# Performance work log

Measured on AMD Instinct MI355X. Metric: run time of the kernel, lower is better.

## Reference

```python
import jax, jax.numpy as jnp
import numpy as np
from jax import lax

B, S = 64, 256          # batch, max sentence length
D, H = 1024, 1024       # encoder hidden (input_dim), LSTM hidden_dim
E, O = 128, 512         # embedding_dim, output_dim (label vocab)
IN = D + E              # lstm_input_dim = input_dim + embedding_dim


def setup_inputs() -> dict:
    key = jax.random.key(0)
    ks = jax.random.split(key, 10)
    u = 1.0 / np.sqrt(H)  # torch LSTM/Linear init scale
    return {
        "hidden": jax.random.normal(ks[0], (B, S, D), jnp.float32),
        "init_tensor": jax.random.normal(ks[1], (1, E), jnp.float32),
        "emb_table": jax.random.normal(ks[2], (O, E), jnp.float32),
        "w_ih": jax.random.uniform(ks[3], (4 * H, IN), jnp.float32, -u, u),
        "w_hh": jax.random.uniform(ks[4], (4 * H, H), jnp.float32, -u, u),
        "b_ih": jax.random.uniform(ks[5], (4 * H,), jnp.float32, -u, u),
        "b_hh": jax.random.uniform(ks[6], (4 * H,), jnp.float32, -u, u),
        "w_out": jax.random.uniform(ks[7], (O, H), jnp.float32, -u, u),
        "b_out": jax.random.uniform(ks[8], (O,), jnp.float32, -u, u),
        "seq_lens": jax.random.randint(ks[9], (B,), 1, S + 1, jnp.int32),
    }


def reference(hidden, init_tensor, emb_table, w_ih, w_hh, b_ih, b_hh,
              w_out, b_out, seq_lens):
    """Autoregressive branch of Seq2SeqDecoder (no teacher forcing):
    per-step LSTM cell -> linear -> argmax -> embedding feedback.
    Dropout is identity (rate 0 / eval). Returns padded [B, S, O] logits,
    zeroed past seq_lens (matching flat2matrix zero padding).
    """
    b = b_ih + b_hh

    def step(carry, x_t):
        h, c, prev_emb = carry                 # [B,H],[B,H],[B,E]
        inp = jnp.concatenate([x_t, prev_emb], axis=-1)       # [B, D+E]
        gates = inp @ w_ih.T + h @ w_hh.T + b                 # [B, 4H]
        i, f, g, o = jnp.split(gates, 4, axis=-1)             # torch gate order
        i, f, o = jax.nn.sigmoid(i), jax.nn.sigmoid(f), jax.nn.sigmoid(o)
        g = jnp.tanh(g)
        c_new = f * c + i * g
        h_new = o * jnp.tanh(c_new)
        logits = h_new @ w_out.T + b_out                      # [B, O]
        idx = jnp.argmax(logits, axis=-1)                     # topk(1)
        return (h_new, c_new, emb_table[idx]), logits

    h0 = jnp.zeros((B, H), hidden.dtype)
    c0 = jnp.zeros((B, H), hidden.dtype)
    e0 = jnp.broadcast_to(init_tensor, (B, E))
    init = (h0, c0, e0)
    _, logits = lax.scan(step, init, jnp.swapaxes(hidden, 0, 1))  # [S,B,O]
    logits = jnp.swapaxes(logits, 0, 1)                            # [B,S,O]
    mask = jnp.arange(S)[None, :] < seq_lens[:, None]              # [B,S]
    return jnp.where(mask[:, :, None], logits, 0.0)
```

## Files before the change

### kernel.cpp

```cpp
#include <hip/hip_runtime.h>
#include <hip/hip_bf16.h>
#include <math.h>

#define B_  64
#define S_  256
#define D_  1024
#define H_  1024
#define E_  128
#define O_  512
#define IN_ 1152
#define G4_ 4096
#define KU_ 1152
#define KS_ 8

__global__ __launch_bounds__(256) void k_init(
    const float* __restrict__ init_tensor,
    const float* __restrict__ w_out,
    float* __restrict__ u, float* __restrict__ c,
    float* __restrict__ w_out_T)
{
  const int NU = B_ * KU_;
  const int NC = B_ * H_;
  const int NT = H_ * O_;
  const int total = NU + NC + NT;
  for (int idx = blockIdx.x * 256 + threadIdx.x; idx < total; idx += gridDim.x * 256) {
    if (idx < NU) {
      int k = idx % KU_;
      u[idx] = (k < E_) ? init_tensor[k] : 0.f;
    } else if (idx < NU + NC) {
      c[idx - NU] = 0.f;
    } else {
      int i = idx - NU - NC;
      int o = i >> 10, k = i & 1023;
      w_out_T[k * O_ + o] = w_out[i];
    }
  }
}

__global__ __launch_bounds__(256) void k_xw(
    const float* __restrict__ hidden,
    const float* __restrict__ w_ih,
    const float* __restrict__ b_ih,
    const float* __restrict__ b_hh,
    float* __restrict__ xwb, int t0, int rows)
{
  __shared__ float a_t[16][132];
  __shared__ float b_t[16][132];
  const int tid = threadIdx.x;
  const int tx = tid & 15, ty = tid >> 4;
  const int m_base = blockIdx.x * 128;
  const int n_base = blockIdx.y * 128;
  float acc[8][8];
#pragma unroll
  for (int i = 0; i < 8; ++i)
#pragma unroll
    for (int j = 0; j < 8; ++j) acc[i][j] = 0.f;

  for (int k0 = 0; k0 < D_; k0 += 16) {
#pragma unroll
    for (int l = 0; l < 2; ++l) {
      int s = tid + l * 256;
      int r = s >> 2, kq = (s & 3) << 2;
      int m = m_base + r;
      float4 v = make_float4(0.f, 0.f, 0.f, 0.f);
      if (m < rows) {
        int t = t0 + (m >> 6), b = m & 63;
        v = *(const float4*)(hidden + ((size_t)b * S_ + t) * D_ + k0 + kq);
      }
      a_t[kq + 0][r] = v.x; a_t[kq + 1][r] = v.y; a_t[kq + 2][r] = v.z; a_t[kq + 3][r] = v.w;
      int j = n_base + r;
      float4 w = *(const float4*)(w_ih + (size_t)j * IN_ + k0 + kq);
      b_t[kq + 0][r] = w.x; b_t[kq + 1][r] = w.y; b_t[kq + 2][r] = w.z; b_t[kq + 3][r] = w.w;
    }
    __syncthreads();
#pragma unroll
    for (int k = 0; k < 16; ++k) {
      float av[8], bv[8];
      *(float4*)&av[0] = *(const float4*)&a_t[k][ty * 4];
      *(float4*)&av[4] = *(const float4*)&a_t[k][64 + ty * 4];
      *(float4*)&bv[0] = *(const float4*)&b_t[k][tx * 4];
      *(float4*)&bv[4] = *(const float4*)&b_t[k][64 + tx * 4];
#pragma unroll
      for (int i = 0; i < 8; ++i)
#pragma unroll
        for (int j = 0; j < 8; ++j)
          acc[i][j] = fmaf(av[i], bv[j], acc[i][j]);
    }
    __syncthreads();
  }
  float bias[8];
#pragma unroll
  for (int cj = 0; cj < 8; ++cj) {
    int col = n_base + ((cj < 4) ? (tx * 4 + cj) : (64 + tx * 4 + cj - 4));
    bias[cj] = b_ih[col] + b_hh[col];
  }
#pragma unroll
  for (int ri = 0; ri < 8; ++ri) {
    int m = m_base + ((ri < 4) ? (ty * 4 + ri) : (64 + ty * 4 + ri - 4));
    if (m < rows) {
      float4 s0 = make_float4(acc[ri][0] + bias[0], acc[ri][1] + bias[1],
                              acc[ri][2] + bias[2], acc[ri][3] + bias[3]);
      float4 s1 = make_float4(acc[ri][4] + bias[4], acc[ri][5] + bias[5],
                              acc[ri][6] + bias[6], acc[ri][7] + bias[7]);
      *(float4*)(xwb + (size_t)m * G4_ + n_base + tx * 4) = s0;
      *(float4*)(xwb + (size_t)m * G4_ + n_base + 64 + tx * 4) = s1;
    }
  }
}

__global__ __launch_bounds__(256) void k_gates(
    const float* __restrict__ u,
    const float* __restrict__ w_ih,
    const float* __restrict__ w_hh,
    float* __restrict__ gp)
{
  __shared__ float u_t[48][68];
  __shared__ float w_t[48][68];
  const int jt = blockIdx.x;
  const int ks = blockIdx.y;
  const int tid = threadIdx.x;
  const int tx = tid & 15, ty = tid >> 4;
  const int j_base = jt * 64;
  float acc[4][4];
#pragma unroll
  for (int i = 0; i < 4; ++i)
#pragma unroll
    for (int j = 0; j < 4; ++j) acc[i][j] = 0.f;

  for (int sub = 0; sub < 3; ++sub) {
    const int k0 = ks * 144 + sub * 48;
#pragma unroll
    for (int l = 0; l < 3; ++l) {
      int s = tid + l * 256;
      int row = s / 12;
      int kq = (s % 12) * 4;
      float4 v = *(const float4*)(u + (size_t)row * KU_ + k0 + kq);
      u_t[kq + 0][row] = v.x; u_t[kq + 1][row] = v.y; u_t[kq + 2][row] = v.z; u_t[kq + 3][row] = v.w;
      int kg = k0 + kq;
      int j = j_base + row;
      const float* src = (kg < E_) ? (w_ih + (size_t)j * IN_ + D_ + kg)
                                   : (w_hh + (size_t)j * H_ + (kg - E_));
      float4 w = *(const float4*)src;
      w_t[kq + 0][row] = w.x; w_t[kq + 1][row] = w.y; w_t[kq + 2][row] = w.z; w_t[kq + 3][row] = w.w;
    }
    __syncthreads();
#pragma unroll 16
    for (int k = 0; k < 48; ++k) {
      float uv[4], wv[4];
      *(float4*)uv = *(const float4*)&u_t[k][ty * 4];
      *(float4*)wv = *(const float4*)&w_t[k][tx * 4];
#pragma unroll
      for (int i = 0; i < 4; ++i)
#pragma unroll
        for (int j = 0; j < 4; ++j)
          acc[i][j] = fmaf(uv[i], wv[j], acc[i][j]);
    }
    __syncthreads();
  }
#pragma unroll
  for (int i = 0; i < 4; ++i) {
    int b = ty * 4 + i;
    *(float4*)(gp + ((size_t)ks * B_ + b) * G4_ + j_base + tx * 4) =
        make_float4(acc[i][0], acc[i][1], acc[i][2], acc[i][3]);
  }
}

__global__ __launch_bounds__(256) void k_cell(
    const float* __restrict__ xwb,
    const float* __restrict__ gp,
    float* __restrict__ u,
    float* __restrict__ c,
    const float* __restrict__ w_out_T,
    float* __restrict__ lp,
    int trel)
{
  __shared__ float h_lds[8][128];
  const int bg = blockIdx.x & 7;
  const int sl = blockIdx.x >> 3;
  const int tid = threadIdx.x;
#pragma unroll
  for (int r = 0; r < 4; ++r) {
    int p = tid + r * 256;
    int bl = p >> 7, jjl = p & 127;
    int b = bg * 8 + bl;
    int jj = sl * 128 + jjl;
    float g4[4];
#pragma unroll
    for (int g = 0; g < 4; ++g) {
      int j = g * H_ + jj;
      float v = xwb[((size_t)trel * B_ + b) * G4_ + j];
#pragma unroll
      for (int s8 = 0; s8 < 8; ++s8)
        v += gp[((size_t)s8 * B_ + b) * G4_ + j];
      g4[g] = v;
    }
    float iv = 1.f / (1.f + expf(-g4[0]));
    float fv = 1.f / (1.f + expf(-g4[1]));
    float gv = tanhf(g4[2]);
    float ov = 1.f / (1.f + expf(-g4[3]));
    float cc = fv * c[(size_t)b * H_ + jj] + iv * gv;
    c[(size_t)b * H_ + jj] = cc;
    float hv = ov * tanhf(cc);
    u[(size_t)b * KU_ + E_ + jj] = hv;
    h_lds[bl][jjl] = hv;
  }
  __syncthreads();
  float a0[8], a1[8];
#pragma unroll
  for (int bl = 0; bl < 8; ++bl) { a0[bl] = 0.f; a1[bl] = 0.f; }
  for (int kc = 0; kc < 128; kc += 4) {
    float hb[8][4];
#pragma unroll
    for (int bl = 0; bl < 8; ++bl)
      *(float4*)hb[bl] = *(const float4*)&h_lds[bl][kc];
#pragma unroll
    for (int kk = 0; kk < 4; ++kk) {
      int krow = sl * 128 + kc + kk;
      float w0 = w_out_T[(size_t)krow * O_ + tid];
      float w1 = w_out_T[(size_t)krow * O_ + tid + 256];
#pragma unroll
      for (int bl = 0; bl < 8; ++bl) {
        a0[bl] = fmaf(hb[bl][kk], w0, a0[bl]);
        a1[bl] = fmaf(hb[bl][kk], w1, a1[bl]);
      }
    }
  }
#pragma unroll
  for (int bl = 0; bl < 8; ++bl) {
    int b = bg * 8 + bl;
    lp[((size_t)sl * B_ + b) * O_ + tid]       = a0[bl];
    lp[((size_t)sl * B_ + b) * O_ + tid + 256] = a1[bl];
  }
}

__global__ __launch_bounds__(256) void k_amax(
    const float* __restrict__ lp,
    const float* __restrict__ b_out,
    const float* __restrict__ emb_table,
    const int* __restrict__ seq_lens,
    float* __restrict__ u,
    float* __restrict__ out,
    int t)
{
  __shared__ float sv[256];
  __shared__ int   si[256];
  const int b = blockIdx.x;
  const int tid = threadIdx.x;
  float v0 = b_out[tid];
  float v1 = b_out[tid + 256];
#pragma unroll
  for (int sl = 0; sl < 8; ++sl) {
    v0 += lp[((size_t)sl * B_ + b) * O_ + tid];
    v1 += lp[((size_t)sl * B_ + b) * O_ + tid + 256];
  }
  int len = seq_lens[b];
  float* orow = out + ((size_t)b * S_ + t) * O_;
  bool live = (t < len);
  orow[tid]       = live ? v0 : 0.f;
  orow[tid + 256] = live ? v1 : 0.f;
  float bv = (v1 > v0) ? v1 : v0;
  int   bi = (v1 > v0) ? (tid + 256) : tid;
  sv[tid] = bv; si[tid] = bi;
  __syncthreads();
  for (int s = 128; s > 0; s >>= 1) {
    if (tid < s) {
      float ov = sv[tid + s]; int oi = si[tid + s];
      if (ov > sv[tid] || (ov == sv[tid] && oi < si[tid])) { sv[tid] = ov; si[tid] = oi; }
    }
    __syncthreads();
  }
  int idx = si[0];
  if (tid < E_) u[(size_t)b * KU_ + tid] = emb_table[(size_t)idx * E_ + tid];
}

extern "C" void kernel_launch(void* const* d_in, const int* in_sizes, int n_in,
                              void* d_out, int out_size, void* d_ws, size_t ws_size,
                              hipStream_t stream) {
  const float* hidden      = (const float*)d_in[0];
  const float* init_tensor = (const float*)d_in[1];
  const float* emb_table   = (const float*)d_in[2];
  const float* w_ih        = (const float*)d_in[3];
  const float* w_hh        = (const float*)d_in[4];
  const float* b_ih        = (const float*)d_in[5];
  const float* b_hh        = (const float*)d_in[6];
  const float* w_out       = (const float*)d_in[7];
  const float* b_out       = (const float*)d_in[8];
  const int*   seq_lens    = (const int*)d_in[9];
  float* out = (float*)d_out;
  float* ws  = (float*)d_ws;

  const size_t U_OFF  = 0;
  const size_t C_OFF  = U_OFF + (size_t)B_ * KU_;
  const size_t GP_OFF = C_OFF + (size_t)B_ * H_;
  const size_t LP_OFF = GP_OFF + (size_t)KS_ * B_ * G4_;
  const size_t WT_OFF = LP_OFF + (size_t)8 * B_ * O_;
  const size_t XW_OFF = WT_OFF + (size_t)H_ * O_;

  long long avail = (long long)(ws_size / 4) - (long long)XW_OFF;
  long long chl = avail / ((long long)B_ * G4_);
  int CH = (int)(chl < 1 ? 1 : (chl > S_ ? S_ : chl));

  k_init<<<dim3(2592), dim3(256), 0, stream>>>(init_tensor, w_out,
                                               ws + U_OFF, ws + C_OFF, ws + WT_OFF);

  for (int t0 = 0; t0 < S_; t0 += CH) {
    int ch = (S_ - t0 < CH) ? (S_ - t0) : CH;
    int rows = ch * B_;
    dim3 pg((rows + 127) / 128, G4_ / 128);
    k_xw<<<pg, dim3(256), 0, stream>>>(hidden, w_ih, b_ih, b_hh, ws + XW_OFF, t0, rows);
    for (int t = t0; t < t0 + ch; ++t) {
      k_gates<<<dim3(64, KS_), dim3(256), 0, stream>>>(ws + U_OFF, w_ih, w_hh, ws + GP_OFF);
      k_cell<<<dim3(64), dim3(256), 0, stream>>>(ws + XW_OFF, ws + GP_OFF, ws + U_OFF,
                                                 ws + C_OFF, ws + WT_OFF, ws + LP_OFF, t - t0);
      k_amax<<<dim3(B_), dim3(256), 0, stream>>>(ws + LP_OFF, b_out, emb_table, seq_lens,
                                                 ws + U_OFF, out, t);
    }
  }
}
```

Measured before the change: 10.40 ms.

## Replace per-step kernel launches with persistent cooperative kernel holding weights in registers

Merges the three per-timestep kernels (gates GEMM, LSTM cell + output projection, argmax + embedding feedback) into one persistent cooperative kernel that loops over timesteps and uses grid.sync between phases. Each block keeps its slice of the recurrent and output weights in registers for the whole sequence, so they are not re-read from memory every step, and the state is stored batch-interleaved in LDS-friendly layout. This removes about 768 kernel launches and the repeated weight traffic, at the cost of two grid-wide barriers per step and heavy register and LDS use, which forces a fixed 256-block, 512-thread launch with two blocks per CU.

```diff
diff --git a/kernel.cpp b/kernel.cpp
--- a/kernel.cpp
+++ b/kernel.cpp
@@ -1,6 +1,9 @@
 #include <hip/hip_runtime.h>
 #include <hip/hip_bf16.h>
+#include <hip/hip_cooperative_groups.h>
 #include <math.h>
+
+namespace cg = cooperative_groups;
 
 #define B_  64
 #define S_  256
@@ -11,28 +14,21 @@
 #define IN_ 1152
 #define G4_ 4096
 #define KU_ 1152
-#define KS_ 8
+#define KW_ 144
+
 
 __global__ __launch_bounds__(256) void k_init(
     const float* __restrict__ init_tensor,
-    const float* __restrict__ w_out,
-    float* __restrict__ u, float* __restrict__ c,
-    float* __restrict__ w_out_T)
+    float* __restrict__ u_g, float* __restrict__ c_g)
 {
-  const int NU = B_ * KU_;
-  const int NC = B_ * H_;
-  const int NT = H_ * O_;
-  const int total = NU + NC + NT;
-  for (int idx = blockIdx.x * 256 + threadIdx.x; idx < total; idx += gridDim.x * 256) {
+  const int NU = 4 * KU_ * 16;
+  const int NC = H_ * B_;
+  for (int idx = blockIdx.x * 256 + threadIdx.x; idx < NU + NC; idx += gridDim.x * 256) {
     if (idx < NU) {
-      int k = idx % KU_;
-      u[idx] = (k < E_) ? init_tensor[k] : 0.f;
-    } else if (idx < NU + NC) {
-      c[idx - NU] = 0.f;
+      int k = (idx >> 4) % KU_;
+      u_g[idx] = (k < E_) ? init_tensor[k] : 0.f;
     } else {
-      int i = idx - NU - NC;
-      int o = i >> 10, k = i & 1023;
-      w_out_T[k * O_ + o] = w_out[i];
+      c_g[idx - NU] = 0.f;
     }
   }
 }
@@ -108,169 +104,162 @@
   }
 }
 
-__global__ __launch_bounds__(256) void k_gates(
-    const float* __restrict__ u,
-    const float* __restrict__ w_ih,
-    const float* __restrict__ w_hh,
-    float* __restrict__ gp)
+__global__ __launch_bounds__(512, 2) void k_steps(
+    const float* __restrict__ w_ih, const float* __restrict__ w_hh,
+    const float* __restrict__ w_out, const float* __restrict__ b_out,
+    const float* __restrict__ emb_table, const int* __restrict__ seq_lens,
+    const float* __restrict__ xwb,
+    float* __restrict__ u_g, float* __restrict__ c_g, float* __restrict__ lp,
+    float* __restrict__ out, int t0, int nsteps)
 {
-  __shared__ float u_t[48][68];
-  __shared__ float w_t[48][68];
-  const int jt = blockIdx.x;
-  const int ks = blockIdx.y;
-  const int tid = threadIdx.x;
-  const int tx = tid & 15, ty = tid >> 4;
-  const int j_base = jt * 64;
-  float acc[4][4];
-#pragma unroll
-  for (int i = 0; i < 4; ++i)
-#pragma unroll
-    for (int j = 0; j < 4; ++j) acc[i][j] = 0.f;
-
-  for (int sub = 0; sub < 3; ++sub) {
-    const int k0 = ks * 144 + sub * 48;
-#pragma unroll
-    for (int l = 0; l < 3; ++l) {
-      int s = tid + l * 256;
-      int row = s / 12;
-      int kq = (s % 12) * 4;
-      float4 v = *(const float4*)(u + (size_t)row * KU_ + k0 + kq);
-      u_t[kq + 0][row] = v.x; u_t[kq + 1][row] = v.y; u_t[kq + 2][row] = v.z; u_t[kq + 3][row] = v.w;
-      int kg = k0 + kq;
-      int j = j_base + row;
-      const float* src = (kg < E_) ? (w_ih + (size_t)j * IN_ + D_ + kg)
-                                   : (w_hh + (size_t)j * H_ + (kg - E_));
-      float4 w = *(const float4*)src;
-      w_t[kq + 0][row] = w.x; w_t[kq + 1][row] = w.y; w_t[kq + 2][row] = w.z; w_t[kq + 3][row] = w.w;
-    }
-    __syncthreads();
-#pragma unroll 16
-    for (int k = 0; k < 48; ++k) {
-      float uv[4], wv[4];
-      *(float4*)uv = *(const float4*)&u_t[k][ty * 4];
-      *(float4*)wv = *(const float4*)&w_t[k][tx * 4];
-#pragma unroll
-      for (int i = 0; i < 4; ++i)
-#pragma unroll
-        for (int j = 0; j < 4; ++j)
-          acc[i][j] = fmaf(uv[i], wv[j], acc[i][j]);
-    }
-    __syncthreads();
-  }
-#pragma unroll
-  for (int i = 0; i < 4; ++i) {
-    int b = ty * 4 + i;
-    *(float4*)(gp + ((size_t)ks * B_ + b) * G4_ + j_base + tx * 4) =
-        make_float4(acc[i][0], acc[i][1], acc[i][2], acc[i][3]);
-  }
-}
-
-__global__ __launch_bounds__(256) void k_cell(
-    const float* __restrict__ xwb,
-    const float* __restrict__ gp,
-    float* __restrict__ u,
-    float* __restrict__ c,
-    const float* __restrict__ w_out_T,
-    float* __restrict__ lp,
-    int trel)
-{
-  __shared__ float h_lds[8][128];
-  const int bg = blockIdx.x & 7;
-  const int sl = blockIdx.x >> 3;
-  const int tid = threadIdx.x;
-#pragma unroll
-  for (int r = 0; r < 4; ++r) {
-    int p = tid + r * 256;
-    int bl = p >> 7, jjl = p & 127;
-    int b = bg * 8 + bl;
-    int jj = sl * 128 + jjl;
-    float g4[4];
-#pragma unroll
-    for (int g = 0; g < 4; ++g) {
-      int j = g * H_ + jj;
-      float v = xwb[((size_t)trel * B_ + b) * G4_ + j];
-#pragma unroll
-      for (int s8 = 0; s8 < 8; ++s8)
-        v += gp[((size_t)s8 * B_ + b) * G4_ + j];
-      g4[g] = v;
-    }
-    float iv = 1.f / (1.f + expf(-g4[0]));
-    float fv = 1.f / (1.f + expf(-g4[1]));
-    float gv = tanhf(g4[2]);
-    float ov = 1.f / (1.f + expf(-g4[3]));
-    float cc = fv * c[(size_t)b * H_ + jj] + iv * gv;
-    c[(size_t)b * H_ + jj] = cc;
-    float hv = ov * tanhf(cc);
-    u[(size_t)b * KU_ + E_ + jj] = hv;
-    h_lds[bl][jjl] = hv;
-  }
-  __syncthreads();
-  float a0[8], a1[8];
-#pragma unroll
-  for (int bl = 0; bl < 8; ++bl) { a0[bl] = 0.f; a1[bl] = 0.f; }
-  for (int kc = 0; kc < 128; kc += 4) {
-    float hb[8][4];
-#pragma unroll
-    for (int bl = 0; bl < 8; ++bl)
-      *(float4*)hb[bl] = *(const float4*)&h_lds[bl][kc];
-#pragma unroll
-    for (int kk = 0; kk < 4; ++kk) {
-      int krow = sl * 128 + kc + kk;
-      float w0 = w_out_T[(size_t)krow * O_ + tid];
-      float w1 = w_out_T[(size_t)krow * O_ + tid + 256];
-#pragma unroll
-      for (int bl = 0; bl < 8; ++bl) {
-        a0[bl] = fmaf(hb[bl][kk], w0, a0[bl]);
-        a1[bl] = fmaf(hb[bl][kk], w1, a1[bl]);
-      }
-    }
-  }
-#pragma unroll
-  for (int bl = 0; bl < 8; ++bl) {
-    int b = bg * 8 + bl;
-    lp[((size_t)sl * B_ + b) * O_ + tid]       = a0[bl];
-    lp[((size_t)sl * B_ + b) * O_ + tid + 256] = a1[bl];
-  }
-}
-
-__global__ __launch_bounds__(256) void k_amax(
-    const float* __restrict__ lp,
-    const float* __restrict__ b_out,
-    const float* __restrict__ emb_table,
-    const int* __restrict__ seq_lens,
-    float* __restrict__ u,
-    float* __restrict__ out,
-    int t)
-{
-  __shared__ float sv[256];
-  __shared__ int   si[256];
-  const int b = blockIdx.x;
-  const int tid = threadIdx.x;
-  float v0 = b_out[tid];
-  float v1 = b_out[tid + 256];
-#pragma unroll
-  for (int sl = 0; sl < 8; ++sl) {
-    v0 += lp[((size_t)sl * B_ + b) * O_ + tid];
-    v1 += lp[((size_t)sl * B_ + b) * O_ + tid + 256];
-  }
-  int len = seq_lens[b];
-  float* orow = out + ((size_t)b * S_ + t) * O_;
-  bool live = (t < len);
-  orow[tid]       = live ? v0 : 0.f;
-  orow[tid + 256] = live ? v1 : 0.f;
-  float bv = (v1 > v0) ? v1 : v0;
-  int   bi = (v1 > v0) ? (tid + 256) : tid;
-  sv[tid] = bv; si[tid] = bi;
-  __syncthreads();
-  for (int s = 128; s > 0; s >>= 1) {
-    if (tid < s) {
-      float ov = sv[tid + s]; int oi = si[tid + s];
-      if (ov > sv[tid] || (ov == sv[tid] && oi < si[tid])) { sv[tid] = ov; si[tid] = oi; }
-    }
-    __syncthreads();
-  }
-  int idx = si[0];
-  if (tid < E_) u[(size_t)b * KU_ + tid] = emb_table[(size_t)idx * E_ + tid];
+  __shared__ float u_lds[KU_ * 16];
+  __shared__ float red[8 * 64 * 20];
+  __shared__ float h_lds[16 * 16];
+
+  const int bid  = blockIdx.x;
+  const int jc   = bid >> 2;
+  const int bgrp = bid & 3;
+  const int tid  = threadIdx.x;
+  const int wave = tid >> 6;
+  const int lane = tid & 63;
+  const int g    = lane >> 4;
+  const int jjl  = lane & 15;
+  const int j    = g * H_ + jc * 16 + jjl;
+
+  float wg[KW_];
+  {
+    const int kbase = wave * KW_;
+#pragma unroll
+    for (int k = 0; k < KW_; ++k) {
+      int kg = kbase + k;
+      wg[k] = (kg < E_) ? w_ih[(size_t)j * IN_ + D_ + kg]
+                        : w_hh[(size_t)j * H_ + (kg - E_)];
+    }
+  }
+  float wo[16];
+#pragma unroll
+  for (int k = 0; k < 16; ++k)
+    wo[k] = w_out[(size_t)tid * H_ + jc * 16 + k];
+
+  float* u_my = u_g + (size_t)bgrp * KU_ * 16;
+
+  cg::grid_group grid = cg::this_grid();
+
+  for (int tt = 0; tt < nsteps; ++tt) {
+    const int t = t0 + tt;
+
+    for (int i = tid; i < KU_ * 4; i += 512)
+      *(float4*)&u_lds[i * 4] = *(const float4*)&u_my[i * 4];
+    __syncthreads();
+
+    float acc[16];
+#pragma unroll
+    for (int b = 0; b < 16; ++b) acc[b] = 0.f;
+    {
+      const float* up = u_lds + wave * KW_ * 16;
+#pragma unroll
+      for (int k = 0; k < KW_; ++k) {
+        float4 u0 = *(const float4*)(up + k * 16 + 0);
+        float4 u1 = *(const float4*)(up + k * 16 + 4);
+        float4 u2 = *(const float4*)(up + k * 16 + 8);
+        float4 u3 = *(const float4*)(up + k * 16 + 12);
+        float wk = wg[k];
+        acc[0]  = fmaf(wk, u0.x, acc[0]);  acc[1]  = fmaf(wk, u0.y, acc[1]);
+        acc[2]  = fmaf(wk, u0.z, acc[2]);  acc[3]  = fmaf(wk, u0.w, acc[3]);
+        acc[4]  = fmaf(wk, u1.x, acc[4]);  acc[5]  = fmaf(wk, u1.y, acc[5]);
+        acc[6]  = fmaf(wk, u1.z, acc[6]);  acc[7]  = fmaf(wk, u1.w, acc[7]);
+        acc[8]  = fmaf(wk, u2.x, acc[8]);  acc[9]  = fmaf(wk, u2.y, acc[9]);
+        acc[10] = fmaf(wk, u2.z, acc[10]); acc[11] = fmaf(wk, u2.w, acc[11]);
+        acc[12] = fmaf(wk, u3.x, acc[12]); acc[13] = fmaf(wk, u3.y, acc[13]);
+        acc[14] = fmaf(wk, u3.z, acc[14]); acc[15] = fmaf(wk, u3.w, acc[15]);
+      }
+    }
+    {
+      float* rp = &red[(wave * 64 + lane) * 20];
+#pragma unroll
+      for (int q = 0; q < 4; ++q)
+        *(float4*)&rp[q * 4] = make_float4(acc[q * 4], acc[q * 4 + 1],
+                                           acc[q * 4 + 2], acc[q * 4 + 3]);
+    }
+    __syncthreads();
+
+    if (tid < 256) {
+      const int jl = tid & 15, bb = tid >> 4;
+      const int b = bgrp * 16 + bb;
+      const int jjg = jc * 16 + jl;
+      float gv[4];
+#pragma unroll
+      for (int gg = 0; gg < 4; ++gg) {
+        float s = xwb[((size_t)tt * B_ + b) * G4_ + gg * H_ + jjg];
+#pragma unroll
+        for (int w = 0; w < 8; ++w)
+          s += red[(w * 64 + gg * 16 + jl) * 20 + bb];
+        gv[gg] = s;
+      }
+      float iv = 1.f / (1.f + expf(-gv[0]));
+      float fv = 1.f / (1.f + expf(-gv[1]));
+      float gg2 = tanhf(gv[2]);
+      float ov = 1.f / (1.f + expf(-gv[3]));
+      float cc = fv * c_g[(size_t)jjg * B_ + b] + iv * gg2;
+      c_g[(size_t)jjg * B_ + b] = cc;
+      float hv = ov * tanhf(cc);
+      u_my[(size_t)(E_ + jjg) * 16 + bb] = hv;
+      h_lds[jl * 16 + bb] = hv;
+    }
+    __syncthreads();
+
+    {
+      float acc2[16];
+#pragma unroll
+      for (int b = 0; b < 16; ++b) acc2[b] = 0.f;
+#pragma unroll
+      for (int k = 0; k < 16; ++k) {
+        float4 h0 = *(const float4*)&h_lds[k * 16 + 0];
+        float4 h1 = *(const float4*)&h_lds[k * 16 + 4];
+        float4 h2 = *(const float4*)&h_lds[k * 16 + 8];
+        float4 h3 = *(const float4*)&h_lds[k * 16 + 12];
+        float wk = wo[k];
+        acc2[0]  = fmaf(wk, h0.x, acc2[0]);  acc2[1]  = fmaf(wk, h0.y, acc2[1]);
+        acc2[2]  = fmaf(wk, h0.z, acc2[2]);  acc2[3]  = fmaf(wk, h0.w, acc2[3]);
+        acc2[4]  = fmaf(wk, h1.x, acc2[4]);  acc2[5]  = fmaf(wk, h1.y, acc2[5]);
+        acc2[6]  = fmaf(wk, h1.z, acc2[6]);  acc2[7]  = fmaf(wk, h1.w, acc2[7]);
+        acc2[8]  = fmaf(wk, h2.x, acc2[8]);  acc2[9]  = fmaf(wk, h2.y, acc2[9]);
+        acc2[10] = fmaf(wk, h2.z, acc2[10]); acc2[11] = fmaf(wk, h2.w, acc2[11]);
+        acc2[12] = fmaf(wk, h3.x, acc2[12]); acc2[13] = fmaf(wk, h3.y, acc2[13]);
+        acc2[14] = fmaf(wk, h3.z, acc2[14]); acc2[15] = fmaf(wk, h3.w, acc2[15]);
+      }
+#pragma unroll
+      for (int bb = 0; bb < 16; ++bb)
+        lp[(((size_t)(bgrp * 16 + bb)) * 64 + jc) * O_ + tid] = acc2[bb];
+    }
+    grid.sync();
+
+    if (bid < B_) {
+      const int b = bid;
+      float v = b_out[tid];
+      const float* lpb = lp + (size_t)b * 64 * O_;
+#pragma unroll 8
+      for (int q = 0; q < 64; ++q) v += lpb[(size_t)q * O_ + tid];
+      int len = seq_lens[b];
+      out[((size_t)b * S_ + t) * O_ + tid] = (t < len) ? v : 0.f;
+      float* sv = red;
+      int*   si = (int*)(red + 512);
+      sv[tid] = v; si[tid] = tid;
+      __syncthreads();
+      for (int s = 256; s > 0; s >>= 1) {
+        if (tid < s) {
+          float ov2 = sv[tid + s]; int oi = si[tid + s];
+          if (ov2 > sv[tid] || (ov2 == sv[tid] && oi < si[tid])) { sv[tid] = ov2; si[tid] = oi; }
+        }
+        __syncthreads();
+      }
+      int idx = si[0];
+      if (tid < E_)
+        u_g[(size_t)(b >> 4) * KU_ * 16 + (size_t)tid * 16 + (b & 15)] =
+            emb_table[(size_t)idx * E_ + tid];
+    }
+    grid.sync();
+  }
 }
 
 extern "C" void kernel_launch(void* const* d_in, const int* in_sizes, int n_in,
@@ -290,30 +279,31 @@
   float* ws  = (float*)d_ws;
 
   const size_t U_OFF  = 0;
-  const size_t C_OFF  = U_OFF + (size_t)B_ * KU_;
-  const size_t GP_OFF = C_OFF + (size_t)B_ * H_;
-  const size_t LP_OFF = GP_OFF + (size_t)KS_ * B_ * G4_;
-  const size_t WT_OFF = LP_OFF + (size_t)8 * B_ * O_;
-  const size_t XW_OFF = WT_OFF + (size_t)H_ * O_;
+  const size_t C_OFF  = U_OFF + (size_t)4 * KU_ * 16;
+  const size_t LP_OFF = C_OFF + (size_t)H_ * B_;
+  const size_t XW_OFF = LP_OFF + (size_t)B_ * 64 * O_;
 
   long long avail = (long long)(ws_size / 4) - (long long)XW_OFF;
   long long chl = avail / ((long long)B_ * G4_);
   int CH = (int)(chl < 1 ? 1 : (chl > S_ ? S_ : chl));
 
-  k_init<<<dim3(2592), dim3(256), 0, stream>>>(init_tensor, w_out,
-                                               ws + U_OFF, ws + C_OFF, ws + WT_OFF);
+  k_init<<<dim3(544), dim3(256), 0, stream>>>(init_tensor, ws + U_OFF, ws + C_OFF);
 
   for (int t0 = 0; t0 < S_; t0 += CH) {
     int ch = (S_ - t0 < CH) ? (S_ - t0) : CH;
     int rows = ch * B_;
     dim3 pg((rows + 127) / 128, G4_ / 128);
     k_xw<<<pg, dim3(256), 0, stream>>>(hidden, w_ih, b_ih, b_hh, ws + XW_OFF, t0, rows);
-    for (int t = t0; t < t0 + ch; ++t) {
-      k_gates<<<dim3(64, KS_), dim3(256), 0, stream>>>(ws + U_OFF, w_ih, w_hh, ws + GP_OFF);
-      k_cell<<<dim3(64), dim3(256), 0, stream>>>(ws + XW_OFF, ws + GP_OFF, ws + U_OFF,
-                                                 ws + C_OFF, ws + WT_OFF, ws + LP_OFF, t - t0);
-      k_amax<<<dim3(B_), dim3(256), 0, stream>>>(ws + LP_OFF, b_out, emb_table, seq_lens,
-                                                 ws + U_OFF, out, t);
-    }
+
+    const float* xwbp = ws + XW_OFF;
+    float* u_p  = ws + U_OFF;
+    float* c_p  = ws + C_OFF;
+    float* lp_p = ws + LP_OFF;
+    int t0v = t0, nst = ch;
+    void* args[] = { (void*)&w_ih, (void*)&w_hh, (void*)&w_out, (void*)&b_out,
+                     (void*)&emb_table, (void*)&seq_lens, (void*)&xwbp,
+                     (void*)&u_p, (void*)&c_p, (void*)&lp_p, (void*)&out,
+                     (void*)&t0v, (void*)&nst };
+    hipLaunchCooperativeKernel((void*)k_steps, dim3(256), dim3(512), args, 0, stream);
   }
 }
```

Measured after the change: 33.16 ms. 219% more time.
